# Kernel optimization log

Hardware: AMD Instinct MI355X
Metric: run time of the kernel (lower is better)

The kernel has to match this reference:

```python
import jax, jax.numpy as jnp
import numpy as np

B, T, I, H = 32768, 50, 2, 32  # batch, seq_len, input_size, hidden_size


def setup_inputs() -> dict:
    key = jax.random.key(0)
    ks = jax.random.split(key, 7)
    return {
        "x": jax.random.normal(ks[0], (B, T, I), dtype=jnp.float32),
        "W_ih": jax.random.normal(ks[1], (4 * H, I), dtype=jnp.float32) * 0.1,
        "W_hh": jax.random.normal(ks[2], (4 * H, H), dtype=jnp.float32) * 0.1,
        "b_ih": jax.random.normal(ks[3], (4 * H,), dtype=jnp.float32) * 0.1,
        "b_hh": jax.random.normal(ks[4], (4 * H,), dtype=jnp.float32) * 0.1,
        "W_out": jax.random.normal(ks[5], (1, H), dtype=jnp.float32) * 0.1,
        "b_out": jax.random.normal(ks[6], (1,), dtype=jnp.float32) * 0.1,
        "h0": jnp.zeros((B, H), dtype=jnp.float32),
        "c0": jnp.zeros((B, H), dtype=jnp.float32),
    }


def reference(x, W_ih, W_hh, b_ih, b_hh, W_out, b_out, h0, c0):
    # Precompute input projection for all timesteps: [B, T, 4H]
    xg = jnp.einsum("bti,gi->btg", x, W_ih) + b_ih + b_hh

    def step(carry, xg_t):
        h, c = carry  # [B, H] each
        gates = xg_t + h @ W_hh.T  # [B, 4H]
        i, f, g, o = jnp.split(gates, 4, axis=-1)  # PyTorch gate order i,f,g,o
        i = jax.nn.sigmoid(i)
        f = jax.nn.sigmoid(f)
        g = jnp.tanh(g)
        o = jax.nn.sigmoid(o)
        c = f * c + i * g
        h = o * jnp.tanh(c)
        return (h, c), h

    (_, _), hs = jax.lax.scan(step, (h0, c0), jnp.swapaxes(xg, 0, 1))  # hs: [T, B, H]
    r_out = jnp.swapaxes(hs, 0, 1)  # [B, T, H]
    results = r_out @ W_out.T + b_out  # [B, T, 1]
    return results.reshape(-1, 50, 1)
```

## Files before the change

### kernel.cpp

```cpp
#include <hip/hip_runtime.h>


#define TS 50
#define XROW 204
#define CL 14.0f
#define WPB 4

typedef short short8 __attribute__((ext_vector_type(8)));
typedef float f32x4 __attribute__((ext_vector_type(4)));
typedef float f32x2 __attribute__((ext_vector_type(2)));

__device__ __forceinline__ float fast_exp2(float x) {
    return __builtin_amdgcn_exp2f(x);
}
__device__ __forceinline__ float fast_rcp(float x) {
    return __builtin_amdgcn_rcpf(x);
}
__device__ __forceinline__ f32x2 pexp(f32x2 z) {
    f32x2 r; r.x = fast_exp2(z.x); r.y = fast_exp2(z.y); return r;
}
__device__ __forceinline__ f32x2 prcp(f32x2 v) {
    f32x2 r; r.x = fast_rcp(v.x); r.y = fast_rcp(v.y); return r;
}
__device__ __forceinline__ f32x2 vmin2(f32x2 v, float s) {
    f32x2 sv = {s, s};
    return __builtin_elementwise_min(v, sv);
}
__device__ __forceinline__ unsigned split_pack(float v) {
    unsigned u   = __float_as_uint(v);
    float    res = v - __uint_as_float(u & 0xffff0000u);
    return __builtin_amdgcn_perm(__float_as_uint(res), u, 0x07060302u);
}
__device__ __forceinline__ unsigned lo_pair(unsigned a, unsigned b) {
    return __builtin_amdgcn_perm(b, a, 0x05040100u);
}
__device__ __forceinline__ unsigned hi_pair(unsigned a, unsigned b) {
    return __builtin_amdgcn_perm(b, a, 0x07060302u);
}
__device__ __forceinline__ void pack2(float a, float b,
                                      unsigned &whi, unsigned &wlo) {
    unsigned h, l;
    asm("v_cvt_pk_bf16_f32 %0, %1, %2" : "=v"(h) : "v"(a), "v"(b));
    float ra = a - __uint_as_float(h << 16);
    float rb = b - __uint_as_float(h & 0xffff0000u);
    asm("v_cvt_pk_bf16_f32 %0, %1, %2" : "=v"(l) : "v"(ra), "v"(rb));
    whi = h; wlo = l;
}

union U4S8 { uint4 v; short8 s; unsigned u[4]; };

__global__ __launch_bounds__(256, 2)
void lsnn_kernel(const float* __restrict__ x,
                 const float* __restrict__ W_ih,
                 const float* __restrict__ W_hh,
                 const float* __restrict__ b_ih,
                 const float* __restrict__ b_hh,
                 const float* __restrict__ W_out,
                 const float* __restrict__ b_out,
                 const float* __restrict__ h0,
                 const float* __restrict__ c0,
                 float* __restrict__ out)
{
    __shared__ __align__(16) unsigned xq[WPB][16 * XROW];
    __shared__ __align__(16) float    out_lds[WPB][16 * TS];

    const int  tid  = threadIdx.x;
    const int  g_w  = tid >> 6;
    const int  lane = tid & 63;
    const int  u0   = lane & 15;
    const int  q    = lane >> 4;
    const long b0   = ((long)blockIdx.x * WPB + g_w) * 16;

    unsigned* xqw = xq[g_w];
    float*    ow  = out_lds[g_w];

    for (int i = lane; i < 800; i += 64) {
        int row = i / 50, t = i - row * 50;
        float2 v = *(const float2*)(x + (b0 + row) * 100 + 2 * t);
        unsigned a0 = split_pack(v.x), a1 = split_pack(v.y);
        uint4 w;
        w.x = a0;
        w.y = a1;
        w.z = lo_pair(a0, a1);
        w.w = 0x3f803f80u;
        *(uint4*)&xqw[row * XROW + 4 * t] = w;
    }

    const float L2E = 1.4426950408889634f;
    const float SG  = 2.0f * L2E;

    short8 Awh[8], Awl[8], Aci[8];
    #pragma unroll
    for (int n = 0; n < 8; ++n) {
        const int   g  = n & 3, ub = n >> 2;
        const float s  = (g == 2) ? SG : -L2E;
        const int   R  = g * 32 + ub * 16 + u0;
        const float* wr = W_hh + R * 32;
        U4S8 uh, ul;
        #pragma unroll
        for (int p = 0; p < 4; ++p) {
            unsigned p0 = split_pack(wr[q * 4 + p]      * s);
            unsigned p1 = split_pack(wr[q * 4 + p + 16] * s);
            uh.u[p] = lo_pair(p0, p1);
            ul.u[p] = hi_pair(p0, p1);
        }
        Awh[n] = uh.s;  Awl[n] = ul.s;
        U4S8 ux;
        if (q == 0) {
            unsigned s0 = split_pack(W_ih[R * 2 + 0] * s);
            unsigned s1 = split_pack(W_ih[R * 2 + 1] * s);
            unsigned sb = split_pack((b_ih[R] + b_hh[R]) * s);
            ux.u[0] = lo_pair(s0, s0);
            ux.u[1] = lo_pair(s1, s1);
            ux.u[2] = hi_pair(s0, s1);
            ux.u[3] = sb;
        } else {
            ux.u[0] = 0u; ux.u[1] = 0u; ux.u[2] = 0u; ux.u[3] = 0u;
        }
        Aci[n] = ux.s;
    }
    short8 Awoh, Awol;
    {
        U4S8 uh, ul;
        #pragma unroll
        for (int p = 0; p < 4; ++p) {
            unsigned p0 = split_pack(W_out[q * 4 + p]);
            unsigned p1 = split_pack(W_out[q * 4 + p + 16]);
            uh.u[p] = lo_pair(p0, p1);
            ul.u[p] = hi_pair(p0, p1);
        }
        Awoh = uh.s;  Awol = ul.s;
    }
    const float bout = b_out[0];

    U4S8 Bhh, Bhl;
    {
        const float* hp = h0 + (b0 + u0) * 32 + q * 4;
        float4 ha = *(const float4*)hp;
        float4 hb = *(const float4*)(hp + 16);
        pack2(ha.x, hb.x, Bhh.u[0], Bhl.u[0]);
        pack2(ha.y, hb.y, Bhh.u[1], Bhl.u[1]);
        pack2(ha.z, hb.z, Bhh.u[2], Bhl.u[2]);
        pack2(ha.w, hb.w, Bhh.u[3], Bhl.u[3]);
    }
    f32x2 cst2[4];
    #pragma unroll
    for (int ub = 0; ub < 2; ++ub)
        #pragma unroll
        for (int rr = 0; rr < 2; ++rr)
            cst2[ub * 2 + rr] =
                *(const f32x2*)(c0 + (b0 + u0) * 32 + ub * 16 + q * 4 + 2 * rr);

    const f32x4 ZV = {0.f, 0.f, 0.f, 0.f};
    const int xbase = u0 * XROW;

    uint4 xw = *(const uint4*)&xqw[xbase];

    if (((blockIdx.x ^ (blockIdx.x >> 8)) & 1) != 0)
        __builtin_amdgcn_s_sleep(35);

    #pragma unroll 1
    for (int t = 0; t < TS; ++t) {
        U4S8 Bx;
        Bx.v = xw;
        if (t + 1 < TS)
            xw = *(const uint4*)&xqw[xbase + 4 * (t + 1)];

        if (t > 0) {
            f32x4 aw = ZV;
            aw = __builtin_amdgcn_mfma_f32_16x16x32_bf16(Awoh, Bhh.s, aw, 0, 0, 0);
            aw = __builtin_amdgcn_mfma_f32_16x16x32_bf16(Awoh, Bhl.s, aw, 0, 0, 0);
            aw = __builtin_amdgcn_mfma_f32_16x16x32_bf16(Awol, Bhh.s, aw, 0, 0, 0);
            if (q == 0) ow[u0 * TS + (t - 1)] = aw[0] + bout;
        }

        f32x4 acc[8];
        #pragma unroll
        for (int n = 0; n < 8; ++n)
            acc[n] = __builtin_amdgcn_mfma_f32_16x16x32_bf16(Aci[n], Bx.s, ZV, 0, 0, 0);
        #pragma unroll
        for (int n = 0; n < 8; ++n) {
            acc[n] = __builtin_amdgcn_mfma_f32_16x16x32_bf16(Awh[n], Bhh.s, acc[n], 0, 0, 0);
            acc[n] = __builtin_amdgcn_mfma_f32_16x16x32_bf16(Awh[n], Bhl.s, acc[n], 0, 0, 0);
            acc[n] = __builtin_amdgcn_mfma_f32_16x16x32_bf16(Awl[n], Bhh.s, acc[n], 0, 0, 0);
        }

        f32x2 Bv2[4], Cv2[4], Ev2[4], P12[4], PP2[4];
        #pragma unroll
        for (int ub = 0; ub < 2; ++ub) {
            #pragma unroll
            for (int rr = 0; rr < 2; ++rr) {
                const int gi = ub * 2 + rr, nb = ub * 4;
                f32x2 zi = {acc[nb + 0][2*rr], acc[nb + 0][2*rr + 1]};
                f32x2 zf = {acc[nb + 1][2*rr], acc[nb + 1][2*rr + 1]};
                f32x2 zg = vmin2((f32x2){acc[nb + 2][2*rr], acc[nb + 2][2*rr + 1]}, CL);
                f32x2 zo = {acc[nb + 3][2*rr], acc[nb + 3][2*rr + 1]};
                f32x2 Av = pexp(zi);
                Bv2[gi]  = pexp(zg);
                Ev2[gi]  = pexp(zf);
                Cv2[gi]  = pexp(zo);
                f32x2 Ap = 1.0f + Av;
                P12[gi] = Ap * Bv2[gi] + Ap;
                PP2[gi] = P12[gi] * Ev2[gi] + P12[gi];
            }
        }
        f32x2 R2[4];
        {
            f32x2 s01 = PP2[0] * PP2[1];
            f32x2 s23 = PP2[2] * PP2[3];
            f32x2 ri  = prcp(s01 * s23);
            f32x2 r01 = s23 * ri;
            f32x2 r23 = s01 * ri;
            R2[0] = PP2[1] * r01;  R2[1] = PP2[0] * r01;
            R2[2] = PP2[3] * r23;  R2[3] = PP2[2] * r23;
        }
        f32x2 Dv2[4], Q2[4];
        #pragma unroll
        for (int gi = 0; gi < 4; ++gi) {
            f32x2 fv = P12[gi] * R2[gi];
            f32x2 t2 = Ev2[gi] * R2[gi] + R2[gi];
            f32x2 ig = Bv2[gi] * t2 - t2;
            f32x2 c  = fv * cst2[gi] + ig;
            cst2[gi] = c;
            f32x2 zc = vmin2(c * SG, CL);
            Dv2[gi] = pexp(zc);
            f32x2 Qp = 1.0f + Cv2[gi];
            Q2[gi]  = Qp * Dv2[gi] + Qp;
        }
        f32x2 RQ2[4];
        {
            f32x2 s01 = Q2[0] * Q2[1];
            f32x2 s23 = Q2[2] * Q2[3];
            f32x2 ri  = prcp(s01 * s23);
            f32x2 r01 = s23 * ri;
            f32x2 r23 = s01 * ri;
            RQ2[0] = Q2[1] * r01;  RQ2[1] = Q2[0] * r01;
            RQ2[2] = Q2[3] * r23;  RQ2[3] = Q2[2] * r23;
        }
        f32x2 H0 = Dv2[0] * RQ2[0] - RQ2[0];
        f32x2 H1 = Dv2[1] * RQ2[1] - RQ2[1];
        f32x2 H2 = Dv2[2] * RQ2[2] - RQ2[2];
        f32x2 H3 = Dv2[3] * RQ2[3] - RQ2[3];
        pack2(H0.x, H2.x, Bhh.u[0], Bhl.u[0]);
        pack2(H0.y, H2.y, Bhh.u[1], Bhl.u[1]);
        pack2(H1.x, H3.x, Bhh.u[2], Bhl.u[2]);
        pack2(H1.y, H3.y, Bhh.u[3], Bhl.u[3]);
    }

    {
        f32x4 aw = {0.f, 0.f, 0.f, 0.f};
        aw = __builtin_amdgcn_mfma_f32_16x16x32_bf16(Awoh, Bhh.s, aw, 0, 0, 0);
        aw = __builtin_amdgcn_mfma_f32_16x16x32_bf16(Awoh, Bhl.s, aw, 0, 0, 0);
        aw = __builtin_amdgcn_mfma_f32_16x16x32_bf16(Awol, Bhh.s, aw, 0, 0, 0);
        if (q == 0) ow[u0 * TS + 49] = aw[0] + bout;
    }

    {
        float4* od = (float4*)(out + b0 * 50);
        const float4* os = (const float4*)ow;
        for (int i = lane; i < 200; i += 64) od[i] = os[i];
    }
}

extern "C" void kernel_launch(void* const* d_in, const int* in_sizes, int n_in,
                              void* d_out, int out_size, void* d_ws, size_t ws_size,
                              hipStream_t stream) {
    const float* x     = (const float*)d_in[0];
    const float* W_ih  = (const float*)d_in[1];
    const float* W_hh  = (const float*)d_in[2];
    const float* b_ih  = (const float*)d_in[3];
    const float* b_hh  = (const float*)d_in[4];
    const float* W_out = (const float*)d_in[5];
    const float* b_out = (const float*)d_in[6];
    const float* h0    = (const float*)d_in[7];
    const float* c0    = (const float*)d_in[8];
    float* out = (float*)d_out;

    dim3 grid(32768 / (16 * WPB)), block(64 * WPB);
    lsnn_kernel<<<grid, block, 0, stream>>>(x, W_ih, W_hh, b_ih, b_hh,
                                            W_out, b_out, h0, c0, out);
}
```

Before: 148.4 us.

## Replace split-bf16 triple MFMAs with single fp16 MFMA per gate tile

Drops the hi/lo bf16 splitting of weights and hidden state and uses one fp16 MFMA per tile, with round-toward-zero packing. This cuts the recurrent-step MFMA count by roughly a factor of three and simplifies the packing of x and h. The x staging in LDS shrinks to one packed word per timestep, with the bias term supplied by a constant 1.0 lane. The trade is lower precision, since fp16 truncation accumulates over 50 recurrent steps and risks tolerance failures.

```diff
diff --git a/kernel.cpp b/kernel.cpp
--- a/kernel.cpp
+++ b/kernel.cpp
@@ -2,11 +2,11 @@
 
 
 #define TS 50
-#define XROW 204
+#define XSTR 51
 #define CL 14.0f
 #define WPB 4
 
-typedef short short8 __attribute__((ext_vector_type(8)));
+typedef _Float16 half8 __attribute__((ext_vector_type(8)));
 typedef float f32x4 __attribute__((ext_vector_type(4)));
 typedef float f32x2 __attribute__((ext_vector_type(2)));
 
@@ -26,28 +26,12 @@
     f32x2 sv = {s, s};
     return __builtin_elementwise_min(v, sv);
 }
-__device__ __forceinline__ unsigned split_pack(float v) {
-    unsigned u   = __float_as_uint(v);
-    float    res = v - __uint_as_float(u & 0xffff0000u);
-    return __builtin_amdgcn_perm(__float_as_uint(res), u, 0x07060302u);
-}
-__device__ __forceinline__ unsigned lo_pair(unsigned a, unsigned b) {
-    return __builtin_amdgcn_perm(b, a, 0x05040100u);
-}
-__device__ __forceinline__ unsigned hi_pair(unsigned a, unsigned b) {
-    return __builtin_amdgcn_perm(b, a, 0x07060302u);
-}
-__device__ __forceinline__ void pack2(float a, float b,
-                                      unsigned &whi, unsigned &wlo) {
-    unsigned h, l;
-    asm("v_cvt_pk_bf16_f32 %0, %1, %2" : "=v"(h) : "v"(a), "v"(b));
-    float ra = a - __uint_as_float(h << 16);
-    float rb = b - __uint_as_float(h & 0xffff0000u);
-    asm("v_cvt_pk_bf16_f32 %0, %1, %2" : "=v"(l) : "v"(ra), "v"(rb));
-    whi = h; wlo = l;
-}
-
-union U4S8 { uint4 v; short8 s; unsigned u[4]; };
+__device__ __forceinline__ unsigned pkrtz(float a, float b) {
+    auto h = __builtin_amdgcn_cvt_pkrtz(a, b);
+    return __builtin_bit_cast(unsigned, h);
+}
+
+union U4H8 { uint4 v; half8 h; unsigned u[4]; };
 
 __global__ __launch_bounds__(256, 2)
 void lsnn_kernel(const float* __restrict__ x,
@@ -61,7 +45,7 @@
                  const float* __restrict__ c0,
                  float* __restrict__ out)
 {
-    __shared__ __align__(16) unsigned xq[WPB][16 * XROW];
+    __shared__ __align__(16) unsigned xq[WPB][16 * XSTR];
     __shared__ __align__(16) float    out_lds[WPB][16 * TS];
 
     const int  tid  = threadIdx.x;
@@ -77,71 +61,45 @@
     for (int i = lane; i < 800; i += 64) {
         int row = i / 50, t = i - row * 50;
         float2 v = *(const float2*)(x + (b0 + row) * 100 + 2 * t);
-        unsigned a0 = split_pack(v.x), a1 = split_pack(v.y);
-        uint4 w;
-        w.x = a0;
-        w.y = a1;
-        w.z = lo_pair(a0, a1);
-        w.w = 0x3f803f80u;
-        *(uint4*)&xqw[row * XROW + 4 * t] = w;
+        xqw[row * XSTR + t] = pkrtz(v.x, v.y);
     }
 
     const float L2E = 1.4426950408889634f;
     const float SG  = 2.0f * L2E;
 
-    short8 Awh[8], Awl[8], Aci[8];
+    U4H8 Aw[8], Aci[8];
     #pragma unroll
     for (int n = 0; n < 8; ++n) {
         const int   g  = n & 3, ub = n >> 2;
         const float s  = (g == 2) ? SG : -L2E;
         const int   R  = g * 32 + ub * 16 + u0;
         const float* wr = W_hh + R * 32;
-        U4S8 uh, ul;
-        #pragma unroll
-        for (int p = 0; p < 4; ++p) {
-            unsigned p0 = split_pack(wr[q * 4 + p]      * s);
-            unsigned p1 = split_pack(wr[q * 4 + p + 16] * s);
-            uh.u[p] = lo_pair(p0, p1);
-            ul.u[p] = hi_pair(p0, p1);
-        }
-        Awh[n] = uh.s;  Awl[n] = ul.s;
-        U4S8 ux;
+        #pragma unroll
+        for (int p = 0; p < 4; ++p)
+            Aw[n].u[p] = pkrtz(wr[q * 4 + p] * s, wr[q * 4 + p + 16] * s);
         if (q == 0) {
-            unsigned s0 = split_pack(W_ih[R * 2 + 0] * s);
-            unsigned s1 = split_pack(W_ih[R * 2 + 1] * s);
-            unsigned sb = split_pack((b_ih[R] + b_hh[R]) * s);
-            ux.u[0] = lo_pair(s0, s0);
-            ux.u[1] = lo_pair(s1, s1);
-            ux.u[2] = hi_pair(s0, s1);
-            ux.u[3] = sb;
+            Aci[n].u[0] = pkrtz(W_ih[R * 2 + 0] * s, W_ih[R * 2 + 1] * s);
+            Aci[n].u[1] = pkrtz((b_ih[R] + b_hh[R]) * s, 0.0f);
+            Aci[n].u[2] = 0u;  Aci[n].u[3] = 0u;
         } else {
-            ux.u[0] = 0u; ux.u[1] = 0u; ux.u[2] = 0u; ux.u[3] = 0u;
-        }
-        Aci[n] = ux.s;
-    }
-    short8 Awoh, Awol;
-    {
-        U4S8 uh, ul;
-        #pragma unroll
-        for (int p = 0; p < 4; ++p) {
-            unsigned p0 = split_pack(W_out[q * 4 + p]);
-            unsigned p1 = split_pack(W_out[q * 4 + p + 16]);
-            uh.u[p] = lo_pair(p0, p1);
-            ul.u[p] = hi_pair(p0, p1);
-        }
-        Awoh = uh.s;  Awol = ul.s;
-    }
+            Aci[n].u[0] = 0u; Aci[n].u[1] = 0u; Aci[n].u[2] = 0u; Aci[n].u[3] = 0u;
+        }
+    }
+    U4H8 Awo;
+    #pragma unroll
+    for (int p = 0; p < 4; ++p)
+        Awo.u[p] = pkrtz(W_out[q * 4 + p], W_out[q * 4 + p + 16]);
     const float bout = b_out[0];
 
-    U4S8 Bhh, Bhl;
+    U4H8 Bh;
     {
         const float* hp = h0 + (b0 + u0) * 32 + q * 4;
         float4 ha = *(const float4*)hp;
         float4 hb = *(const float4*)(hp + 16);
-        pack2(ha.x, hb.x, Bhh.u[0], Bhl.u[0]);
-        pack2(ha.y, hb.y, Bhh.u[1], Bhl.u[1]);
-        pack2(ha.z, hb.z, Bhh.u[2], Bhl.u[2]);
-        pack2(ha.w, hb.w, Bhh.u[3], Bhl.u[3]);
+        Bh.u[0] = pkrtz(ha.x, hb.x);
+        Bh.u[1] = pkrtz(ha.y, hb.y);
+        Bh.u[2] = pkrtz(ha.z, hb.z);
+        Bh.u[3] = pkrtz(ha.w, hb.w);
     }
     f32x2 cst2[4];
     #pragma unroll
@@ -152,38 +110,34 @@
                 *(const f32x2*)(c0 + (b0 + u0) * 32 + ub * 16 + q * 4 + 2 * rr);
 
     const f32x4 ZV = {0.f, 0.f, 0.f, 0.f};
-    const int xbase = u0 * XROW;
-
-    uint4 xw = *(const uint4*)&xqw[xbase];
+    const int xbase = u0 * XSTR;
+
+    unsigned xw = xqw[xbase];
 
     if (((blockIdx.x ^ (blockIdx.x >> 8)) & 1) != 0)
         __builtin_amdgcn_s_sleep(35);
 
     #pragma unroll 1
     for (int t = 0; t < TS; ++t) {
-        U4S8 Bx;
-        Bx.v = xw;
+        U4H8 Bx;
+        Bx.u[0] = xw;
+        Bx.u[1] = 0x00003c00u;
+        Bx.u[2] = 0u;  Bx.u[3] = 0u;
         if (t + 1 < TS)
-            xw = *(const uint4*)&xqw[xbase + 4 * (t + 1)];
+            xw = xqw[xbase + t + 1];
 
         if (t > 0) {
-            f32x4 aw = ZV;
-            aw = __builtin_amdgcn_mfma_f32_16x16x32_bf16(Awoh, Bhh.s, aw, 0, 0, 0);
-            aw = __builtin_amdgcn_mfma_f32_16x16x32_bf16(Awoh, Bhl.s, aw, 0, 0, 0);
-            aw = __builtin_amdgcn_mfma_f32_16x16x32_bf16(Awol, Bhh.s, aw, 0, 0, 0);
+            f32x4 aw = __builtin_amdgcn_mfma_f32_16x16x32_f16(Awo.h, Bh.h, ZV, 0, 0, 0);
             if (q == 0) ow[u0 * TS + (t - 1)] = aw[0] + bout;
         }
 
         f32x4 acc[8];
         #pragma unroll
         for (int n = 0; n < 8; ++n)
-            acc[n] = __builtin_amdgcn_mfma_f32_16x16x32_bf16(Aci[n], Bx.s, ZV, 0, 0, 0);
-        #pragma unroll
-        for (int n = 0; n < 8; ++n) {
-            acc[n] = __builtin_amdgcn_mfma_f32_16x16x32_bf16(Awh[n], Bhh.s, acc[n], 0, 0, 0);
-            acc[n] = __builtin_amdgcn_mfma_f32_16x16x32_bf16(Awh[n], Bhl.s, acc[n], 0, 0, 0);
-            acc[n] = __builtin_amdgcn_mfma_f32_16x16x32_bf16(Awl[n], Bhh.s, acc[n], 0, 0, 0);
-        }
+            acc[n] = __builtin_amdgcn_mfma_f32_16x16x32_f16(Aci[n].h, Bx.h, ZV, 0, 0, 0);
+        #pragma unroll
+        for (int n = 0; n < 8; ++n)
+            acc[n] = __builtin_amdgcn_mfma_f32_16x16x32_f16(Aw[n].h, Bh.h, acc[n], 0, 0, 0);
 
         f32x2 Bv2[4], Cv2[4], Ev2[4], P12[4], PP2[4];
         #pragma unroll
@@ -241,17 +195,14 @@
         f32x2 H1 = Dv2[1] * RQ2[1] - RQ2[1];
         f32x2 H2 = Dv2[2] * RQ2[2] - RQ2[2];
         f32x2 H3 = Dv2[3] * RQ2[3] - RQ2[3];
-        pack2(H0.x, H2.x, Bhh.u[0], Bhl.u[0]);
-        pack2(H0.y, H2.y, Bhh.u[1], Bhl.u[1]);
-        pack2(H1.x, H3.x, Bhh.u[2], Bhl.u[2]);
-        pack2(H1.y, H3.y, Bhh.u[3], Bhl.u[3]);
+        Bh.u[0] = pkrtz(H0.x, H2.x);
+        Bh.u[1] = pkrtz(H0.y, H2.y);
+        Bh.u[2] = pkrtz(H1.x, H3.x);
+        Bh.u[3] = pkrtz(H1.y, H3.y);
     }
 
     {
-        f32x4 aw = {0.f, 0.f, 0.f, 0.f};
-        aw = __builtin_amdgcn_mfma_f32_16x16x32_bf16(Awoh, Bhh.s, aw, 0, 0, 0);
-        aw = __builtin_amdgcn_mfma_f32_16x16x32_bf16(Awoh, Bhl.s, aw, 0, 0, 0);
-        aw = __builtin_amdgcn_mfma_f32_16x16x32_bf16(Awol, Bhh.s, aw, 0, 0, 0);
+        f32x4 aw = __builtin_amdgcn_mfma_f32_16x16x32_f16(Awo.h, Bh.h, ZV, 0, 0, 0);
         if (q == 0) ow[u0 * TS + 49] = aw[0] + bout;
     }
 
```

Measured after the change: 135.6 us. 1.09x faster.
